# Optimization experiments

Measured on AMD Instinct MI355X. Metric: run time of the kernel, lower is better.

## Reference

```python
import jax, jax.numpy as jnp
import numpy as np
from jax import lax

HIDDEN = 16
DN = ('NCHW', 'OIHW', 'NCHW')

def setup_inputs() -> dict:
    key = jax.random.key(0)
    k1, k2, k3 = jax.random.split(key, 3)
    b, t, c, h, w = 8, 12, 5, 256, 256
    x = jax.random.normal(k1, (b, t, c, h, w), dtype=jnp.float32)
    # PyTorch-like init scale for conv weights
    W_cell = jax.random.normal(k2, (4 * HIDDEN, c + HIDDEN, 3, 3), dtype=jnp.float32) * 0.05
    b_cell = jnp.zeros((4 * HIDDEN,), dtype=jnp.float32)
    W_final = jax.random.normal(k3, (1, HIDDEN, 1, 1), dtype=jnp.float32) * 0.1
    b_final = jnp.zeros((1,), dtype=jnp.float32)
    return {"x": x, "W_cell": W_cell, "b_cell": b_cell,
            "W_final": W_final, "b_final": b_final}

def _cell_step(h_c, x_t, W_cell, b_cell):
    h_cur, c_cur = h_c
    combined = jnp.concatenate([x_t, h_cur], axis=1)          # [B, C+H, H, W]
    conv = lax.conv_general_dilated(combined, W_cell, (1, 1), 'SAME',
                                    dimension_numbers=DN)
    conv = conv + b_cell[None, :, None, None]                  # [B, 4H, H, W]
    cc_i, cc_f, cc_o, cc_g = jnp.split(conv, 4, axis=1)
    i = jax.nn.sigmoid(cc_i)
    f = jax.nn.sigmoid(cc_f)
    o = jax.nn.sigmoid(cc_o)
    g = jnp.tanh(cc_g)
    c_next = f * c_cur + i * g
    h_next = o * jnp.tanh(c_next)
    return h_next, c_next

def reference(x, W_cell, b_cell, W_final, b_final):
    b, t, c, hh, ww = x.shape
    h0 = jnp.zeros((b, HIDDEN, hh, ww), dtype=x.dtype)
    c0 = jnp.zeros((b, HIDDEN, hh, ww), dtype=x.dtype)
    xt = jnp.moveaxis(x, 1, 0)  # [T, B, C, H, W] for scan over time

    def step(carry, x_t):
        return _cell_step(carry, x_t, W_cell, b_cell), None

    (h_last, _), _ = lax.scan(step, (h0, c0), xt)
    out = lax.conv_general_dilated(h_last, W_final, (1, 1), 'SAME',
                                   dimension_numbers=DN)
    out = out + b_final[None, :, None, None]
    return out
```

## Files before the change

kernel.cpp:

```cpp
#include <hip/hip_runtime.h>
#include <math.h>

#define HIDDEN 16
#define CIN 5
#define BB 8
#define TT 12
#define HH 256
#define WW 256
#define TX 32
#define TY 8
#define HALO_X 34
#define HALO_Y 10
#define NPX (HALO_X * HALO_Y)
#define STRIDE 40
#define PTX 32
#define PTY 4
#define PHX 34
#define PHY 6
#define PNPX (PHX * PHY)
#define ROWSH 24
#define NTILES 4096
#define NBLK_PERSIST 1024
#define XSTEP (HH * WW * 8)
#define WSH (9 * 4 * 48 * 8)
#define WSH_PAD (WSH + 8)
#define TILE_SH (PNPX * ROWSH)
#define WOFF TILE_SH
#define ZOFF (TILE_SH + WSH)
#define SMSH (TILE_SH + WSH_PAD)

typedef __attribute__((ext_vector_type(8))) short bf16x8;
typedef __attribute__((ext_vector_type(4))) float floatx4;

__device__ __forceinline__ unsigned short f2bf(float f) {
    unsigned int u = __float_as_uint(f);
    u += 0x7fffu + ((u >> 16) & 1u);
    return (unsigned short)(u >> 16);
}
__device__ __forceinline__ float bf2f(unsigned short s) {
    return __uint_as_float(((unsigned int)s) << 16);
}
__device__ __forceinline__ float rcpf(float x) {
    float r;
    asm("v_rcp_f32 %0, %1" : "=v"(r) : "v"(x));
    return r;
}
__device__ __forceinline__ float fast_sigmoid(float x) {
    return rcpf(1.0f + __expf(-x));
}
__device__ __forceinline__ float fast_tanh(float x) {
    float e2 = __expf(-2.0f * fabsf(x));
    float t = (1.0f - e2) * rcpf(1.0f + e2);
    return copysignf(t, x);
}
__device__ __forceinline__ float leg_sigmoid(float x) { return 1.0f / (1.0f + __expf(-x)); }
__device__ __forceinline__ float leg_tanh(float x) {
    float e2 = __expf(-2.0f * fabsf(x));
    float t = (1.0f - e2) / (1.0f + e2);
    return copysignf(t, x);
}

__global__ void prep_w_kernel(const float* __restrict__ Wc,
                              unsigned short* __restrict__ Wfrag) {
    int i = blockIdx.x * 256 + threadIdx.x;
    if (i >= WSH_PAD) return;
    if (i >= WSH) { Wfrag[i] = 0; return; }
    int j    = i & 7;
    int t8   = i >> 3;
    int lane = t8 % 48;
    int t48  = t8 / 48;
    int g    = t48 & 3;
    int tap  = t48 >> 2;
    int k    = ((lane >> 4) << 3) + j;
    int col  = lane & 15;
    int o    = g * 16 + col;
    float w  = 0.0f;
    if (k < 21) {
        int ci_ref = (k < 16) ? (5 + k) : (k - 16);
        w = Wc[(o * 21 + ci_ref) * 9 + tap];
    }
    Wfrag[i] = f2bf(w);
}

__global__ void prep_x_kernel(const float* __restrict__ x,
                              unsigned short* __restrict__ xp) {
    size_t n = (size_t)blockIdx.x * 256 + threadIdx.x;
    const size_t TOTPX = (size_t)BB * TT * HH * WW;
    if (n >= TOTPX) return;
    size_t bt  = n / (size_t)(HH * WW);
    size_t pix = n - bt * (size_t)(HH * WW);
    const float* src = x + bt * (size_t)CIN * HH * WW + pix;
    unsigned short v[8];
    #pragma unroll
    for (int c = 0; c < CIN; ++c) v[c] = f2bf(src[(size_t)c * HH * WW]);
    v[5] = 0; v[6] = 0; v[7] = 0;
    *(uint4*)&xp[n * 8] = *(const uint4*)v;
}

__global__ void prep_flags_kernel(unsigned int* __restrict__ flags) {
    int i = blockIdx.x * 256 + threadIdx.x;
    if (i < NTILES) flags[i] = 0;
}

__global__ __launch_bounds__(256, 4)
void convlstm_persistent_kernel(const float* __restrict__ x,
                                const unsigned short* __restrict__ xp,
                                unsigned short* __restrict__ ha,
                                unsigned short* __restrict__ hbuf,
                                const unsigned short* __restrict__ Wfrag,
                                const float* __restrict__ bias,
                                const float* __restrict__ Wf,
                                const float* __restrict__ bfin,
                                float* __restrict__ out,
                                unsigned int* __restrict__ flags,
                                int use_xp) {
    __shared__ unsigned short sm[SMSH];

    const int tid  = threadIdx.x;
    const int lane = tid & 63;
    const int wave = tid >> 6;
    const int u    = lane & 15;
    const int quad = lane >> 4;
    const int bid  = (int)blockIdx.x;

    const int bb = bid >> 7;
    const int ty = (bid >> 1) & 63;
    const int y0 = ty * PTY;
    const int n0 = bid * 4;

    for (int i = tid; i < WSH_PAD / 8; i += 256)
        *(uint4*)&sm[WOFF + i * 8] = *(const uint4*)&Wfrag[i * 8];

    const int wbl   = (lane < 48) ? (WOFF + lane * 8) : ZOFF;
    const int wstep = (lane < 48) ? 384 : 0;

    int nb_dy = 0, nb_dx = 0;
    {
        int s  = lane + (lane >= 4 ? 1 : 0);
        nb_dy = s / 3 - 1;
        nb_dx = s - (s / 3) * 3 - 1;
    }

    const int sly = tid / PHX;
    const int slx = tid - sly * PHX;
    const int gy  = y0 + sly - 1;
    const bool yok = (gy >= 0) && (gy < HH);
    const int hbase_y = (bb * HH * WW + gy * WW) * HIDDEN;
    const int xbase_y = (bb * TT * HH * WW + gy * WW) * 8;

    float bg[4];
    #pragma unroll
    for (int g = 0; g < 4; ++g) bg[g] = bias[g * 16 + u];
    const float wfu = Wf[u];
    const float bf0 = bfin[0];

    int A[2];
    #pragma unroll
    for (int mh = 0; mh < 2; ++mh)
        A[mh] = (quad < 3) ? ((wave * PHX + mh * 16 + u) * ROWSH + quad * 8)
                           : ZOFF;
    const int msel = (quad < 3) ? ROWSH : 0;

    float cV0[2][4], cV1[2][4], cV2[2][4], cV3[2][4];
    #pragma unroll
    for (int m = 0; m < 2; ++m)
        #pragma unroll
        for (int r = 0; r < 4; ++r) {
            cV0[m][r] = 0.0f; cV1[m][r] = 0.0f;
            cV2[m][r] = 0.0f; cV3[m][r] = 0.0f;
        }

    #pragma unroll 1
    for (int t = 0; t < TT; ++t) {
        const unsigned short* h_in  = (t & 1) ? ha : hbuf;
        unsigned short*       h_out = (t & 1) ? hbuf : ha;
        const int first = (t == 0);
        const int last  = (t == TT - 1);

        #pragma unroll 1
        for (int v = 0; v < 4; ++v) {
            const int n  = n0 + v;
            const int tx = n & 7;
            const int x0 = tx * PTX;

            if (t > 0) {
                if (wave == 0) {
                    bool act = (lane < 8) && (tx + nb_dx >= 0) && (tx + nb_dx < 8)
                                          && (ty + nb_dy >= 0) && (ty + nb_dy < 64);
                    int nb = n + nb_dy * 8 + nb_dx;
                    const unsigned need = (unsigned)t;
                    for (;;) {
                        unsigned fv = act
                            ? __hip_atomic_load(&flags[nb], __ATOMIC_RELAXED,
                                                __HIP_MEMORY_SCOPE_AGENT)
                            : 0xFFFFFFFFu;
                        if (__all(fv >= need)) break;
                        __builtin_amdgcn_s_sleep(2);
                    }
                    if (tid == 0) __threadfence();
                }
                __syncthreads();
            }

            if (tid < PNPX) {
                unsigned short* row = &sm[tid * ROWSH];
                uint4 z = {0, 0, 0, 0};
                int gx = x0 + slx - 1;
                bool inb = yok && ((unsigned)gx < (unsigned)WW);
                if (inb && !first) {
                    const unsigned short* hp = h_in + hbase_y + gx * HIDDEN;
                    *(uint4*)&row[0] = *(const uint4*)&hp[0];
                    *(uint4*)&row[8] = *(const uint4*)&hp[8];
                } else {
                    *(uint4*)&row[0] = z;
                    *(uint4*)&row[8] = z;
                }
                if (use_xp) {
                    if (inb)
                        *(uint4*)&row[16] =
                            *(const uint4*)&xp[xbase_y + t * XSTEP + gx * 8];
                    else
                        *(uint4*)&row[16] = z;
                } else {
                    unsigned short vv[8];
                    #pragma unroll
                    for (int ci = 0; ci < CIN; ++ci) {
                        float f = 0.0f;
                        if (inb) f = x[(((size_t)bb * TT + t) * CIN + ci)
                                       * (size_t)(HH * WW) + gy * WW + gx];
                        vv[ci] = f2bf(f);
                    }
                    vv[5] = 0; vv[6] = 0; vv[7] = 0;
                    *(uint4*)&row[16] = *(const uint4*)vv;
                }
            }
            __syncthreads();

            floatx4 acc[2][4];
            #pragma unroll
            for (int mh = 0; mh < 2; ++mh)
                #pragma unroll
                for (int g = 0; g < 4; ++g)
                    acc[mh][g] = (floatx4){bg[g], bg[g], bg[g], bg[g]};

            #pragma unroll 3
            for (int tap = 0; tap < 9; ++tap) {
                int ky = tap / 3;
                int kx = tap - ky * 3;
                int ktap = ky * PHX + kx;
                bf16x8 bfr[4];
                #pragma unroll
                for (int g = 0; g < 4; ++g)
                    bfr[g] = *(const bf16x8*)&sm[wbl + (tap * 4 + g) * wstep];
                #pragma unroll
                for (int mh = 0; mh < 2; ++mh) {
                    bf16x8 af = *(const bf16x8*)&sm[A[mh] + ktap * msel];
                    #pragma unroll
                    for (int g = 0; g < 4; ++g)
                        acc[mh][g] = __builtin_amdgcn_mfma_f32_16x16x32_bf16(
                            af, bfr[g], acc[mh][g], 0, 0, 0);
                }
            }

            #pragma unroll
            for (int mh = 0; mh < 2; ++mh) {
                int py = y0 + wave;
                int col0 = mh * 16 + quad * 4;
                size_t gidx0 = ((size_t)bb * HH * WW + (size_t)py * WW + x0 + col0)
                               * HIDDEN + u;
                #pragma unroll
                for (int r = 0; r < 4; ++r) {
                    float ig = fast_sigmoid(acc[mh][0][r]);
                    float fg = fast_sigmoid(acc[mh][1][r]);
                    float og = fast_sigmoid(acc[mh][2][r]);
                    float gg = fast_tanh(acc[mh][3][r]);
                    float c_old = (v & 2) ? ((v & 1) ? cV3[mh][r] : cV2[mh][r])
                                          : ((v & 1) ? cV1[mh][r] : cV0[mh][r]);
                    float c_new = fg * c_old + ig * gg;
                    if (v & 2) { if (v & 1) cV3[mh][r] = c_new; else cV2[mh][r] = c_new; }
                    else       { if (v & 1) cV1[mh][r] = c_new; else cV0[mh][r] = c_new; }
                    float hval = og * fast_tanh(c_new);
                    if (last) {
                        float s = wfu * hval;
                        s += __shfl_xor(s, 1);
                        s += __shfl_xor(s, 2);
                        s += __shfl_xor(s, 4);
                        s += __shfl_xor(s, 8);
                        if (u == 0)
                            out[(size_t)bb * HH * WW + (size_t)py * WW + x0 + col0 + r]
                                = s + bf0;
                    } else {
                        h_out[gidx0 + (size_t)r * HIDDEN] = f2bf(hval);
                    }
                }
            }

            __syncthreads();
            if (!last && tid == 0) {
                __threadfence();
                __hip_atomic_store(&flags[n], (unsigned)(t + 1), __ATOMIC_RELAXED,
                                   __HIP_MEMORY_SCOPE_AGENT);
            }
        }
    }
}

__global__ __launch_bounds__(256, 5)
void convlstm_step_kernel(const float* __restrict__ x, int t,
                          const unsigned short* __restrict__ xp,
                          const unsigned short* __restrict__ h_in,
                          unsigned short* __restrict__ h_out,
                          float* __restrict__ c_state,
                          const unsigned short* __restrict__ Wfrag,
                          const float* __restrict__ bias,
                          int first, int use_xp) {
    __shared__ unsigned short tile[NPX * STRIDE];

    const int tid  = threadIdx.x;
    const int lane = tid & 63;
    const int wave = tid >> 6;
    const int x0 = blockIdx.x * TX;
    const int y0 = blockIdx.y * TY;
    const int bb = blockIdx.z;

    for (int i = tid; i < NPX; i += 256) {
        int ly = i / HALO_X;
        int lx = i - ly * HALO_X;
        int gy = y0 + ly - 1;
        int gx = x0 + lx - 1;
        bool inb = (gy >= 0 && gy < HH && gx >= 0 && gx < WW);
        unsigned short* row = &tile[i * STRIDE];
        uint4 z = {0, 0, 0, 0};
        if (inb && !first) {
            size_t hbase = ((size_t)bb * HH * WW + (size_t)gy * WW + gx) * HIDDEN;
            *(uint4*)&row[0] = *(const uint4*)&h_in[hbase];
            *(uint4*)&row[8] = *(const uint4*)&h_in[hbase + 8];
        } else {
            *(uint4*)&row[0] = z;
            *(uint4*)&row[8] = z;
        }
        if (use_xp) {
            if (inb) {
                size_t xb = (((size_t)bb * TT + t) * (size_t)(HH * WW)
                             + (size_t)gy * WW + gx) * 8;
                *(uint4*)&row[16] = *(const uint4*)&xp[xb];
            } else {
                *(uint4*)&row[16] = z;
            }
        } else {
            #pragma unroll
            for (int ci = 0; ci < CIN; ++ci) {
                float v = 0.0f;
                if (inb) v = x[(((size_t)bb * TT + t) * CIN + ci) * (size_t)(HH * WW)
                               + (size_t)gy * WW + gx];
                row[16 + ci] = f2bf(v);
            }
            row[21] = 0; row[22] = 0; row[23] = 0;
        }
        *(uint4*)&row[24] = z;
    }
    __syncthreads();

    const int u    = lane & 15;
    const int quad = lane >> 4;

    const unsigned short* wptr = (lane < 48) ? (Wfrag + lane * 8) : (Wfrag + WSH);
    const int wstep2 = (lane < 48) ? 384 : 0;

    float bg[4];
    #pragma unroll
    for (int g = 0; g < 4; ++g) bg[g] = bias[g * 16 + u];

    #pragma unroll 1
    for (int half = 0; half < 2; ++half) {
        floatx4 acc[2][4];
        int abase[2];
        #pragma unroll
        for (int mh = 0; mh < 2; ++mh) {
            int ml = half * 2 + mh;
            int m  = wave + ml * 4;
            int my = m >> 1;
            int mx = (m & 1) << 4;
            abase[mh] = (my * HALO_X + mx + u) * STRIDE + quad * 8;
            #pragma unroll
            for (int g = 0; g < 4; ++g)
                acc[mh][g] = (floatx4){bg[g], bg[g], bg[g], bg[g]};
        }

        #pragma unroll 3
        for (int tap = 0; tap < 9; ++tap) {
            int ky = tap / 3;
            int kx = tap - ky * 3;
            int toff = (ky * HALO_X + kx) * STRIDE;
            bf16x8 bfr[4];
            #pragma unroll
            for (int g = 0; g < 4; ++g)
                bfr[g] = *(const bf16x8*)&wptr[(tap * 4 + g) * wstep2];
            #pragma unroll
            for (int mh = 0; mh < 2; ++mh) {
                bf16x8 af = *(const bf16x8*)&tile[abase[mh] + toff];
                #pragma unroll
                for (int g = 0; g < 4; ++g)
                    acc[mh][g] = __builtin_amdgcn_mfma_f32_16x16x32_bf16(
                        af, bfr[g], acc[mh][g], 0, 0, 0);
            }
        }

        #pragma unroll
        for (int mh = 0; mh < 2; ++mh) {
            int ml = half * 2 + mh;
            int m  = wave + ml * 4;
            int my = m >> 1;
            int mx = (m & 1) << 4;
            int py = y0 + my;
            #pragma unroll
            for (int r = 0; r < 4; ++r) {
                int pxx = x0 + mx + quad * 4 + r;
                size_t idx = ((size_t)bb * HH * WW + (size_t)py * WW + pxx) * HIDDEN + u;
                float ig = leg_sigmoid(acc[mh][0][r]);
                float fg = leg_sigmoid(acc[mh][1][r]);
                float og = leg_sigmoid(acc[mh][2][r]);
                float gg = leg_tanh(acc[mh][3][r]);
                float c_old = first ? 0.0f : c_state[idx];
                float c_new = fg * c_old + ig * gg;
                c_state[idx] = c_new;
                h_out[idx] = f2bf(og * leg_tanh(c_new));
            }
        }
    }
}

__global__ void final_conv_kernel(const unsigned short* __restrict__ h,
                                  const float* __restrict__ Wf,
                                  const float* __restrict__ bf_,
                                  float* __restrict__ out) {
    int i = blockIdx.x * 256 + threadIdx.x;
    if (i >= BB * HH * WW) return;
    size_t base = (size_t)i * HIDDEN;
    uint4 v0 = *(const uint4*)&h[base];
    uint4 v1 = *(const uint4*)&h[base + 8];
    const unsigned short* p0 = (const unsigned short*)&v0;
    const unsigned short* p1 = (const unsigned short*)&v1;
    float s = bf_[0];
    #pragma unroll
    for (int k = 0; k < 8; ++k) s += Wf[k] * bf2f(p0[k]);
    #pragma unroll
    for (int k = 0; k < 8; ++k) s += Wf[8 + k] * bf2f(p1[k]);
    out[i] = s;
}

extern "C" void kernel_launch(void* const* d_in, const int* in_sizes, int n_in,
                              void* d_out, int out_size, void* d_ws, size_t ws_size,
                              hipStream_t stream) {
    const float* x  = (const float*)d_in[0];
    const float* Wc = (const float*)d_in[1];
    const float* bc = (const float*)d_in[2];
    const float* Wf = (const float*)d_in[3];
    const float* bf = (const float*)d_in[4];
    float* out = (float*)d_out;

    char* ws = (char*)d_ws;
    const size_t h_bytes = (size_t)BB * HH * WW * HIDDEN * 2;
    const size_t c_bytes = (size_t)BB * HH * WW * HIDDEN * 4;
    const size_t w_bytes = (size_t)WSH_PAD * 2;
    const size_t f_bytes = (size_t)NTILES * 4;
    const size_t x_bytes = (size_t)BB * TT * HH * WW * 8 * 2;

    unsigned short* h_a = (unsigned short*)(ws);
    unsigned short* h_b = (unsigned short*)(ws + h_bytes);
    float* c            = (float*)(ws + 2 * h_bytes);
    unsigned short* Wfr = (unsigned short*)(ws + 2 * h_bytes + c_bytes);
    unsigned int* flags = (unsigned int*)(ws + 2 * h_bytes + c_bytes + w_bytes);
    unsigned short* xp  = (unsigned short*)(ws + 2 * h_bytes + c_bytes + w_bytes + f_bytes);

    const int use_xp =
        (ws_size >= 2 * h_bytes + c_bytes + w_bytes + f_bytes + x_bytes) ? 1 : 0;

    prep_w_kernel<<<(WSH_PAD + 255) / 256, 256, 0, stream>>>(Wc, Wfr);
    prep_flags_kernel<<<(NTILES + 255) / 256, 256, 0, stream>>>(flags);
    if (use_xp) {
        size_t totpx = (size_t)BB * TT * HH * WW;
        prep_x_kernel<<<(int)((totpx + 255) / 256), 256, 0, stream>>>(x, xp);
    }

    int occ = 0;
    hipOccupancyMaxActiveBlocksPerMultiprocessor(&occ, convlstm_persistent_kernel,
                                                 256, 0);
    bool done = false;
    if (occ >= 4) {
        const unsigned short* xp_arg = use_xp ? xp : (const unsigned short*)0;
        int use_xp_arg = use_xp;
        void* kargs[] = {
            (void*)&x, (void*)&xp_arg, (void*)&h_a, (void*)&h_b,
            (void*)&Wfr, (void*)&bc, (void*)&Wf, (void*)&bf,
            (void*)&out, (void*)&flags, (void*)&use_xp_arg
        };
        if (hipLaunchCooperativeKernel((const void*)convlstm_persistent_kernel,
                                       dim3(NBLK_PERSIST, 1, 1), dim3(256, 1, 1),
                                       kargs, 0, stream) == hipSuccess)
            done = true;
    }

    if (!done) {
        dim3 grid(WW / TX, HH / TY, BB);
        dim3 block(256, 1, 1);
        const unsigned short* h_in = h_a;
        for (int t = 0; t < TT; ++t) {
            unsigned short* h_out = (t & 1) ? h_b : h_a;
            convlstm_step_kernel<<<grid, block, 0, stream>>>(
                x, t, use_xp ? xp : (const unsigned short*)0,
                h_in, h_out, c, Wfr, bc, (t == 0) ? 1 : 0, use_xp);
            h_in = h_out;
        }
        final_conv_kernel<<<(BB * HH * WW + 255) / 256, 256, 0, stream>>>(
            h_in, Wf, bf, out);
    }
}
```

Before: 715.5 us.

## Hold conv weights in registers and enlarge persistent tiles to 64x8

The persistent ConvLSTM kernel now loads all 36 bf16 weight fragments into VGPRs once per block instead of reading them from shared memory each tap. Tiles grow from 32x4 to 64x8 pixels, with 512 blocks at two per CU handling two tiles each. This cuts halo overhead and neighbour-flag syncs. Because register-resident cell state no longer fits, c is now read from and written to global memory every timestep. The trade is register pressure and lower occupancy against extra global traffic for c.

After: 685.8 us. 4.1% less time.

```diff
diff --git a/kernel.cpp b/kernel.cpp
--- a/kernel.cpp
+++ b/kernel.cpp
@@ -13,21 +13,18 @@
 #define HALO_Y 10
 #define NPX (HALO_X * HALO_Y)
 #define STRIDE 40
-#define PTX 32
-#define PTY 4
-#define PHX 34
-#define PHY 6
+#define PTX 64
+#define PTY 8
+#define PHX 66
+#define PHY 10
 #define PNPX (PHX * PHY)
-#define ROWSH 24
-#define NTILES 4096
-#define NBLK_PERSIST 1024
+#define ROWSH 28
+#define ZOFF (PNPX * ROWSH)
+#define SMSH (ZOFF + 8)
+#define NTILES 1024
+#define NBLK 512
 #define XSTEP (HH * WW * 8)
-#define WSH (9 * 4 * 48 * 8)
-#define WSH_PAD (WSH + 8)
-#define TILE_SH (PNPX * ROWSH)
-#define WOFF TILE_SH
-#define ZOFF (TILE_SH + WSH)
-#define SMSH (TILE_SH + WSH_PAD)
+#define WTAB (9 * 4 * 64 * 8)
 
 typedef __attribute__((ext_vector_type(8))) short bf16x8;
 typedef __attribute__((ext_vector_type(4))) float floatx4;
@@ -63,14 +60,11 @@
 __global__ void prep_w_kernel(const float* __restrict__ Wc,
                               unsigned short* __restrict__ Wfrag) {
     int i = blockIdx.x * 256 + threadIdx.x;
-    if (i >= WSH_PAD) return;
-    if (i >= WSH) { Wfrag[i] = 0; return; }
+    if (i >= WTAB) return;
     int j    = i & 7;
-    int t8   = i >> 3;
-    int lane = t8 % 48;
-    int t48  = t8 / 48;
-    int g    = t48 & 3;
-    int tap  = t48 >> 2;
+    int lane = (i >> 3) & 63;
+    int g    = (i >> 9) & 3;
+    int tap  = i >> 11;
     int k    = ((lane >> 4) << 3) + j;
     int col  = lane & 15;
     int o    = g * 16 + col;
@@ -102,18 +96,17 @@
     if (i < NTILES) flags[i] = 0;
 }
 
-__global__ __launch_bounds__(256, 4)
-void convlstm_persistent_kernel(const float* __restrict__ x,
-                                const unsigned short* __restrict__ xp,
-                                unsigned short* __restrict__ ha,
-                                unsigned short* __restrict__ hbuf,
-                                const unsigned short* __restrict__ Wfrag,
-                                const float* __restrict__ bias,
-                                const float* __restrict__ Wf,
-                                const float* __restrict__ bfin,
-                                float* __restrict__ out,
-                                unsigned int* __restrict__ flags,
-                                int use_xp) {
+__global__ __launch_bounds__(256, 2)
+void convlstm_wreg_kernel(const unsigned short* __restrict__ xp,
+                          unsigned short* __restrict__ ha,
+                          unsigned short* __restrict__ hb,
+                          float* __restrict__ c_state,
+                          const unsigned short* __restrict__ Wfrag,
+                          const float* __restrict__ bias,
+                          const float* __restrict__ Wf,
+                          const float* __restrict__ bfin,
+                          float* __restrict__ out,
+                          unsigned int* __restrict__ flags) {
     __shared__ unsigned short sm[SMSH];
 
     const int tid  = threadIdx.x;
@@ -123,78 +116,74 @@
     const int quad = lane >> 4;
     const int bid  = (int)blockIdx.x;
 
-    const int bb = bid >> 7;
-    const int ty = (bid >> 1) & 63;
-    const int y0 = ty * PTY;
-    const int n0 = bid * 4;
-
-    for (int i = tid; i < WSH_PAD / 8; i += 256)
-        *(uint4*)&sm[WOFF + i * 8] = *(const uint4*)&Wfrag[i * 8];
-
-    const int wbl   = (lane < 48) ? (WOFF + lane * 8) : ZOFF;
-    const int wstep = (lane < 48) ? 384 : 0;
+    const int n0  = bid * 2;
+    const int bb  = n0 >> 7;
+    const int rem = n0 & 127;
+    const int ty  = rem >> 2;
+    const int tx0 = rem & 3;
+    const int y0  = ty * PTY;
+
+    bf16x8 wreg[36];
+    #pragma unroll
+    for (int i = 0; i < 36; ++i)
+        wreg[i] = *(const bf16x8*)&Wfrag[(size_t)(i * 64 + lane) * 8];
+
+    if (tid == 0) { uint4 z = {0, 0, 0, 0}; *(uint4*)&sm[ZOFF] = z; }
 
     int nb_dy = 0, nb_dx = 0;
     {
-        int s  = lane + (lane >= 4 ? 1 : 0);
-        nb_dy = s / 3 - 1;
-        nb_dx = s - (s / 3) * 3 - 1;
-    }
-
-    const int sly = tid / PHX;
-    const int slx = tid - sly * PHX;
-    const int gy  = y0 + sly - 1;
-    const bool yok = (gy >= 0) && (gy < HH);
-    const int hbase_y = (bb * HH * WW + gy * WW) * HIDDEN;
-    const int xbase_y = (bb * TT * HH * WW + gy * WW) * 8;
+        int s8 = lane + (lane >= 4 ? 1 : 0);
+        nb_dy = s8 / 3 - 1;
+        nb_dx = s8 - (s8 / 3) * 3 - 1;
+    }
+
+    int scol[3], hby[3], xby[3];
+    bool sval[3], yok[3];
+    #pragma unroll
+    for (int it = 0; it < 3; ++it) {
+        int i = tid + it * 256;
+        sval[it] = (i < PNPX);
+        int ly = i / PHX;
+        int lx = i - ly * PHX;
+        int gy = y0 + ly - 1;
+        yok[it]  = ((unsigned)gy < (unsigned)HH);
+        scol[it] = lx - 1;
+        hby[it]  = (bb * HH * WW + gy * WW) * HIDDEN;
+        xby[it]  = (bb * TT * HH * WW + gy * WW) * 8;
+    }
 
     float bg[4];
     #pragma unroll
     for (int g = 0; g < 4; ++g) bg[g] = bias[g * 16 + u];
     const float wfu = Wf[u];
     const float bf0 = bfin[0];
-
-    int A[2];
-    #pragma unroll
-    for (int mh = 0; mh < 2; ++mh)
-        A[mh] = (quad < 3) ? ((wave * PHX + mh * 16 + u) * ROWSH + quad * 8)
-                           : ZOFF;
-    const int msel = (quad < 3) ? ROWSH : 0;
-
-    float cV0[2][4], cV1[2][4], cV2[2][4], cV3[2][4];
-    #pragma unroll
-    for (int m = 0; m < 2; ++m)
-        #pragma unroll
-        for (int r = 0; r < 4; ++r) {
-            cV0[m][r] = 0.0f; cV1[m][r] = 0.0f;
-            cV2[m][r] = 0.0f; cV3[m][r] = 0.0f;
-        }
+    const int msel  = (quad < 3) ? ROWSH : 0;
 
     #pragma unroll 1
     for (int t = 0; t < TT; ++t) {
-        const unsigned short* h_in  = (t & 1) ? ha : hbuf;
-        unsigned short*       h_out = (t & 1) ? hbuf : ha;
+        const unsigned short* h_in = (t & 1) ? ha : hb;
+        unsigned short* h_out      = (t & 1) ? hb : ha;
         const int first = (t == 0);
         const int last  = (t == TT - 1);
 
         #pragma unroll 1
-        for (int v = 0; v < 4; ++v) {
+        for (int v = 0; v < 2; ++v) {
             const int n  = n0 + v;
-            const int tx = n & 7;
+            const int tx = tx0 + v;
             const int x0 = tx * PTX;
 
             if (t > 0) {
                 if (wave == 0) {
-                    bool act = (lane < 8) && (tx + nb_dx >= 0) && (tx + nb_dx < 8)
-                                          && (ty + nb_dy >= 0) && (ty + nb_dy < 64);
-                    int nb = n + nb_dy * 8 + nb_dx;
-                    const unsigned need = (unsigned)t;
+                    bool act = (lane < 8)
+                        && ((unsigned)(tx + nb_dx) < 4u)
+                        && ((unsigned)(ty + nb_dy) < 32u);
+                    int nb = n + nb_dy * 4 + nb_dx;
                     for (;;) {
                         unsigned fv = act
                             ? __hip_atomic_load(&flags[nb], __ATOMIC_RELAXED,
                                                 __HIP_MEMORY_SCOPE_AGENT)
                             : 0xFFFFFFFFu;
-                        if (__all(fv >= need)) break;
+                        if (__all(fv >= (unsigned)t)) break;
                         __builtin_amdgcn_s_sleep(2);
                     }
                     if (tid == 0) __threadfence();
@@ -202,95 +191,90 @@
                 __syncthreads();
             }
 
-            if (tid < PNPX) {
-                unsigned short* row = &sm[tid * ROWSH];
-                uint4 z = {0, 0, 0, 0};
-                int gx = x0 + slx - 1;
-                bool inb = yok && ((unsigned)gx < (unsigned)WW);
-                if (inb && !first) {
-                    const unsigned short* hp = h_in + hbase_y + gx * HIDDEN;
-                    *(uint4*)&row[0] = *(const uint4*)&hp[0];
-                    *(uint4*)&row[8] = *(const uint4*)&hp[8];
-                } else {
-                    *(uint4*)&row[0] = z;
-                    *(uint4*)&row[8] = z;
+            #pragma unroll
+            for (int it = 0; it < 3; ++it) {
+                if (sval[it]) {
+                    unsigned short* rp = &sm[(tid + it * 256) * ROWSH];
+                    uint4 z = {0, 0, 0, 0};
+                    int gx = x0 + scol[it];
+                    bool inb = yok[it] && ((unsigned)gx < (unsigned)WW);
+                    if (inb && !first) {
+                        const unsigned short* hp = h_in + hby[it] + gx * HIDDEN;
+                        *(uint4*)&rp[0] = *(const uint4*)&hp[0];
+                        *(uint4*)&rp[8] = *(const uint4*)&hp[8];
+                    } else {
+                        *(uint4*)&rp[0] = z; *(uint4*)&rp[8] = z;
+                    }
+                    if (inb)
+                        *(uint4*)&rp[16] =
+                            *(const uint4*)&xp[xby[it] + t * XSTEP + gx * 8];
+                    else
+                        *(uint4*)&rp[16] = z;
                 }
-                if (use_xp) {
-                    if (inb)
-                        *(uint4*)&row[16] =
-                            *(const uint4*)&xp[xbase_y + t * XSTEP + gx * 8];
-                    else
-                        *(uint4*)&row[16] = z;
-                } else {
-                    unsigned short vv[8];
-                    #pragma unroll
-                    for (int ci = 0; ci < CIN; ++ci) {
-                        float f = 0.0f;
-                        if (inb) f = x[(((size_t)bb * TT + t) * CIN + ci)
-                                       * (size_t)(HH * WW) + gy * WW + gx];
-                        vv[ci] = f2bf(f);
-                    }
-                    vv[5] = 0; vv[6] = 0; vv[7] = 0;
-                    *(uint4*)&row[16] = *(const uint4*)vv;
-                }
             }
             __syncthreads();
 
-            floatx4 acc[2][4];
-            #pragma unroll
-            for (int mh = 0; mh < 2; ++mh)
-                #pragma unroll
-                for (int g = 0; g < 4; ++g)
-                    acc[mh][g] = (floatx4){bg[g], bg[g], bg[g], bg[g]};
-
-            #pragma unroll 3
-            for (int tap = 0; tap < 9; ++tap) {
-                int ky = tap / 3;
-                int kx = tap - ky * 3;
-                int ktap = ky * PHX + kx;
-                bf16x8 bfr[4];
-                #pragma unroll
-                for (int g = 0; g < 4; ++g)
-                    bfr[g] = *(const bf16x8*)&sm[wbl + (tap * 4 + g) * wstep];
+            #pragma unroll 1
+            for (int hh = 0; hh < 4; ++hh) {
+                floatx4 acc[2][4];
+                int A[2];
                 #pragma unroll
                 for (int mh = 0; mh < 2; ++mh) {
-                    bf16x8 af = *(const bf16x8*)&sm[A[mh] + ktap * msel];
+                    int m   = wave * 8 + hh * 2 + mh;
+                    int my  = m >> 2;
+                    int mxt = m & 3;
+                    A[mh] = (quad < 3)
+                        ? ((my * PHX + mxt * 16 + u) * ROWSH + quad * 8) : ZOFF;
                     #pragma unroll
                     for (int g = 0; g < 4; ++g)
-                        acc[mh][g] = __builtin_amdgcn_mfma_f32_16x16x32_bf16(
-                            af, bfr[g], acc[mh][g], 0, 0, 0);
+                        acc[mh][g] = (floatx4){bg[g], bg[g], bg[g], bg[g]};
                 }
-            }
-
-            #pragma unroll
-            for (int mh = 0; mh < 2; ++mh) {
-                int py = y0 + wave;
-                int col0 = mh * 16 + quad * 4;
-                size_t gidx0 = ((size_t)bb * HH * WW + (size_t)py * WW + x0 + col0)
-                               * HIDDEN + u;
+
                 #pragma unroll
-                for (int r = 0; r < 4; ++r) {
-                    float ig = fast_sigmoid(acc[mh][0][r]);
-                    float fg = fast_sigmoid(acc[mh][1][r]);
-                    float og = fast_sigmoid(acc[mh][2][r]);
-                    float gg = fast_tanh(acc[mh][3][r]);
-                    float c_old = (v & 2) ? ((v & 1) ? cV3[mh][r] : cV2[mh][r])
-                                          : ((v & 1) ? cV1[mh][r] : cV0[mh][r]);
-                    float c_new = fg * c_old + ig * gg;
-                    if (v & 2) { if (v & 1) cV3[mh][r] = c_new; else cV2[mh][r] = c_new; }
-                    else       { if (v & 1) cV1[mh][r] = c_new; else cV0[mh][r] = c_new; }
-                    float hval = og * fast_tanh(c_new);
-                    if (last) {
-                        float s = wfu * hval;
-                        s += __shfl_xor(s, 1);
-                        s += __shfl_xor(s, 2);
-                        s += __shfl_xor(s, 4);
-                        s += __shfl_xor(s, 8);
-                        if (u == 0)
-                            out[(size_t)bb * HH * WW + (size_t)py * WW + x0 + col0 + r]
-                                = s + bf0;
-                    } else {
-                        h_out[gidx0 + (size_t)r * HIDDEN] = f2bf(hval);
+                for (int tap = 0; tap < 9; ++tap) {
+                    int ktap = (tap / 3) * PHX + (tap % 3);
+                    #pragma unroll
+                    for (int mh = 0; mh < 2; ++mh) {
+                        bf16x8 af = *(const bf16x8*)&sm[A[mh] + ktap * msel];
+                        #pragma unroll
+                        for (int g = 0; g < 4; ++g)
+                            acc[mh][g] = __builtin_amdgcn_mfma_f32_16x16x32_bf16(
+                                af, wreg[tap * 4 + g], acc[mh][g], 0, 0, 0);
+                    }
+                }
+
+                #pragma unroll
+                for (int mh = 0; mh < 2; ++mh) {
+                    int m   = wave * 8 + hh * 2 + mh;
+                    int my  = m >> 2;
+                    int mxt = m & 3;
+                    int py  = y0 + my;
+                    int col0 = mxt * 16 + quad * 4;
+                    size_t gidx0 = ((size_t)bb * HH * WW + (size_t)py * WW + x0 + col0)
+                                   * HIDDEN + u;
+                    #pragma unroll
+                    for (int r = 0; r < 4; ++r) {
+                        float ig = fast_sigmoid(acc[mh][0][r]);
+                        float fg = fast_sigmoid(acc[mh][1][r]);
+                        float og = fast_sigmoid(acc[mh][2][r]);
+                        float gg = fast_tanh(acc[mh][3][r]);
+                        size_t gidx = gidx0 + (size_t)r * HIDDEN;
+                        float c_old = first ? 0.0f : c_state[gidx];
+                        float c_new = fg * c_old + ig * gg;
+                        float hval = og * fast_tanh(c_new);
+                        if (last) {
+                            float sred = wfu * hval;
+                            sred += __shfl_xor(sred, 1);
+                            sred += __shfl_xor(sred, 2);
+                            sred += __shfl_xor(sred, 4);
+                            sred += __shfl_xor(sred, 8);
+                            if (u == 0)
+                                out[(size_t)bb * HH * WW + (size_t)py * WW
+                                    + x0 + col0 + r] = sred + bf0;
+                        } else {
+                            c_state[gidx] = c_new;
+                            h_out[gidx] = f2bf(hval);
+                        }
                     }
                 }
             }
@@ -364,9 +348,6 @@
     const int u    = lane & 15;
     const int quad = lane >> 4;
 
-    const unsigned short* wptr = (lane < 48) ? (Wfrag + lane * 8) : (Wfrag + WSH);
-    const int wstep2 = (lane < 48) ? 384 : 0;
-
     float bg[4];
     #pragma unroll
     for (int g = 0; g < 4; ++g) bg[g] = bias[g * 16 + u];
@@ -395,7 +376,7 @@
             bf16x8 bfr[4];
             #pragma unroll
             for (int g = 0; g < 4; ++g)
-                bfr[g] = *(const bf16x8*)&wptr[(tap * 4 + g) * wstep2];
+                bfr[g] = *(const bf16x8*)&Wfrag[(size_t)((tap * 4 + g) * 64 + lane) * 8];
             #pragma unroll
             for (int mh = 0; mh < 2; ++mh) {
                 bf16x8 af = *(const bf16x8*)&tile[abase[mh] + toff];
@@ -462,7 +443,7 @@
     char* ws = (char*)d_ws;
     const size_t h_bytes = (size_t)BB * HH * WW * HIDDEN * 2;
     const size_t c_bytes = (size_t)BB * HH * WW * HIDDEN * 4;
-    const size_t w_bytes = (size_t)WSH_PAD * 2;
+    const size_t w_bytes = (size_t)WTAB * 2;
     const size_t f_bytes = (size_t)NTILES * 4;
     const size_t x_bytes = (size_t)BB * TT * HH * WW * 8 * 2;
 
@@ -473,32 +454,32 @@
     unsigned int* flags = (unsigned int*)(ws + 2 * h_bytes + c_bytes + w_bytes);
     unsigned short* xp  = (unsigned short*)(ws + 2 * h_bytes + c_bytes + w_bytes + f_bytes);
 
-    const int use_xp =
+    const int have_xp =
         (ws_size >= 2 * h_bytes + c_bytes + w_bytes + f_bytes + x_bytes) ? 1 : 0;
 
-    prep_w_kernel<<<(WSH_PAD + 255) / 256, 256, 0, stream>>>(Wc, Wfr);
+    prep_w_kernel<<<(WTAB + 255) / 256, 256, 0, stream>>>(Wc, Wfr);
     prep_flags_kernel<<<(NTILES + 255) / 256, 256, 0, stream>>>(flags);
-    if (use_xp) {
+    if (have_xp) {
         size_t totpx = (size_t)BB * TT * HH * WW;
         prep_x_kernel<<<(int)((totpx + 255) / 256), 256, 0, stream>>>(x, xp);
     }
 
-    int occ = 0;
-    hipOccupancyMaxActiveBlocksPerMultiprocessor(&occ, convlstm_persistent_kernel,
-                                                 256, 0);
     bool done = false;
-    if (occ >= 4) {
-        const unsigned short* xp_arg = use_xp ? xp : (const unsigned short*)0;
-        int use_xp_arg = use_xp;
-        void* kargs[] = {
-            (void*)&x, (void*)&xp_arg, (void*)&h_a, (void*)&h_b,
-            (void*)&Wfr, (void*)&bc, (void*)&Wf, (void*)&bf,
-            (void*)&out, (void*)&flags, (void*)&use_xp_arg
-        };
-        if (hipLaunchCooperativeKernel((const void*)convlstm_persistent_kernel,
-                                       dim3(NBLK_PERSIST, 1, 1), dim3(256, 1, 1),
-                                       kargs, 0, stream) == hipSuccess)
-            done = true;
+    if (have_xp) {
+        int occ = 0;
+        hipOccupancyMaxActiveBlocksPerMultiprocessor(&occ, convlstm_wreg_kernel,
+                                                     256, 0);
+        if (occ >= 2) {
+            void* kargs[] = {
+                (void*)&xp, (void*)&h_a, (void*)&h_b, (void*)&c,
+                (void*)&Wfr, (void*)&bc, (void*)&Wf, (void*)&bf,
+                (void*)&out, (void*)&flags
+            };
+            if (hipLaunchCooperativeKernel((const void*)convlstm_wreg_kernel,
+                                           dim3(NBLK, 1, 1), dim3(256, 1, 1),
+                                           kargs, 0, stream) == hipSuccess)
+                done = true;
+        }
     }
 
     if (!done) {
@@ -508,8 +489,8 @@
         for (int t = 0; t < TT; ++t) {
             unsigned short* h_out = (t & 1) ? h_b : h_a;
             convlstm_step_kernel<<<grid, block, 0, stream>>>(
-                x, t, use_xp ? xp : (const unsigned short*)0,
-                h_in, h_out, c, Wfr, bc, (t == 0) ? 1 : 0, use_xp);
+                x, t, have_xp ? xp : (const unsigned short*)0,
+                h_in, h_out, c, Wfr, bc, (t == 0) ? 1 : 0, have_xp);
             h_in = h_out;
         }
         final_conv_kernel<<<(BB * HH * WW + 255) / 256, 256, 0, stream>>>(
```
